# Kernel optimization log

Hardware: AMD Instinct MI355X
Metric: run time of the kernel (lower is better)

The kernel has to match this reference:

```python
import jax, jax.numpy as jnp
import numpy as np


def setup_inputs() -> dict:
    key = jax.random.key(0)
    kq, kk, kv = jax.random.split(key, 3)
    B, H, S, D = 2, 16, 2048, 64
    return {
        "queries": jax.random.normal(kq, (B, H, S, D), dtype=jnp.float32),
        "keys": jax.random.normal(kk, (B, H, S, D), dtype=jnp.float32),
        "values": jax.random.normal(kv, (B, H, S, D), dtype=jnp.float32),
        "d_k": D,
    }


def reference(queries, keys, values, d_k):
    # scores = Q K^T / sqrt(d_k)  -> [B, H, S, S]
    scale = 1.0 / jnp.sqrt(jnp.asarray(d_k, dtype=queries.dtype))
    scores = jnp.einsum("bhqd,bhkd->bhqk", queries, keys) * scale
    weights = jax.nn.softmax(scores, axis=-1)
    return jnp.einsum("bhqk,bhkd->bhqd", weights, values)
```

## Files before the change

### kernel.cpp

```cpp
#include <hip/hip_runtime.h>


typedef _Float16 half8 __attribute__((ext_vector_type(8)));
typedef _Float16 half4 __attribute__((ext_vector_type(4)));
typedef __fp16 fp16x2 __attribute__((ext_vector_type(2)));
typedef float floatx4 __attribute__((ext_vector_type(4)));

constexpr int BQ = 128;
constexpr int BK = 64;
constexpr int DH = 64;
constexpr int SLEN = 2048;
constexpr int NT = SLEN / BK;
constexpr int THREADS = 256;

#define MFMA16(a, b, c) __builtin_amdgcn_mfma_f32_16x16x32_f16(a, b, c, 0, 0, 0)

static __device__ __forceinline__ void load_lds16(const _Float16* g, _Float16* l) {
    __builtin_amdgcn_global_load_lds(
        (const __attribute__((address_space(1))) void*)g,
        (__attribute__((address_space(3))) void*)l, 16, 0, 0);
}

__global__ __launch_bounds__(256)
void prep_frags(const float* __restrict__ K, const float* __restrict__ V,
                _Float16* __restrict__ F)
{
    __shared__ _Float16 kt_[64 * 72];
    __shared__ _Float16 vt_[64 * 72];
    const int tid  = threadIdx.x;
    const int tile = blockIdx.x & 31;
    const int head = blockIdx.x >> 5;
    const size_t base = ((size_t)head * SLEN + tile * 64) * DH;
    const float4* Ks = (const float4*)(K + base);
    const float4* Vs = (const float4*)(V + base);
    #pragma unroll
    for (int r = 0; r < 4; r++) {
        int i = tid + 256 * r, row = i >> 4, g = i & 15;
        float4 a = Ks[row * 16 + g];
        half4 h;
        h[0] = (_Float16)a.x; h[1] = (_Float16)a.y;
        h[2] = (_Float16)a.z; h[3] = (_Float16)a.w;
        *(half4*)&kt_[row * 72 + g * 4] = h;
        float4 b = Vs[row * 16 + g];
        half4 h2;
        h2[0] = (_Float16)b.x; h2[1] = (_Float16)b.y;
        h2[2] = (_Float16)b.z; h2[3] = (_Float16)b.w;
        *(half4*)&vt_[row * 72 + g * 4] = h2;
    }
    __syncthreads();
    _Float16* dst = F + (size_t)(head * 32 + tile) * 8192;
    #pragma unroll
    for (int r = 0; r < 2; r++) {
        int s = tid + 256 * r;
        int frag = s >> 6, lane = s & 63;
        int kd = frag >> 2, c = frag & 3;
        int quad = lane >> 4, n16 = lane & 15;
        int key = (c >> 1) * 32 + (c & 1) * 4 + (n16 >> 2) * 8 + (n16 & 3);
        *(half8*)&dst[s * 8] = *(const half8*)&kt_[key * 72 + kd * 32 + quad * 8];
    }
    #pragma unroll
    for (int r = 0; r < 2; r++) {
        int s = tid + 256 * r;
        int frag = s >> 6, lane = s & 63;
        int kd2 = frag >> 2, c2 = frag & 3;
        int quad = lane >> 4, n16 = lane & 15;
        int d = c2 * 16 + n16;
        int key0 = kd2 * 32 + quad * 8;
        half8 h;
        #pragma unroll
        for (int j = 0; j < 8; j++) h[j] = vt_[(key0 + j) * 72 + d];
        *(half8*)&dst[4096 + s * 8] = h;
    }
}

__global__ __launch_bounds__(THREADS, 2)
void attn_f16_mfma(const float* __restrict__ Q, const _Float16* __restrict__ F,
                   float* __restrict__ Out, const int* __restrict__ dkp)
{
    __shared__ _Float16 lds[2][8192];

    const int tid  = threadIdx.x;
    const int wq   = tid >> 6;
    const int lane = tid & 63;
    const int quad = lane >> 4;
    const int n16  = lane & 15;

    const int id   = blockIdx.x;
    const int xcd  = id & 7;
    const int slot = id >> 3;
    const int head = xcd * 4 + (slot >> 4);
    const int qt   = slot & 15;

    const float scale2 = rsqrtf((float)(*dkp)) * 1.44269504088896340736f;
    const size_t headoff = (size_t)head * SLEN * DH;

    half8 qB[2][2];
    {
        const float4* Qg = (const float4*)(Q + headoff + (size_t)(qt * BQ + wq * 32) * DH);
        #pragma unroll
        for (int rg = 0; rg < 2; rg++)
            #pragma unroll
            for (int kd = 0; kd < 2; kd++) {
                int row = rg * 16 + n16;
                float4 a = Qg[row * 16 + kd * 8 + quad * 2];
                float4 b = Qg[row * 16 + kd * 8 + quad * 2 + 1];
                half8 h;
                h[0] = (_Float16)(a.x * scale2); h[1] = (_Float16)(a.y * scale2);
                h[2] = (_Float16)(a.z * scale2); h[3] = (_Float16)(a.w * scale2);
                h[4] = (_Float16)(b.x * scale2); h[5] = (_Float16)(b.y * scale2);
                h[6] = (_Float16)(b.z * scale2); h[7] = (_Float16)(b.w * scale2);
                qB[rg][kd] = h;
            }
    }

    const _Float16* Fh = F + (size_t)head * 32 * 8192;

    auto stage = [&](int b, int kt) {
        const _Float16* src = Fh + (size_t)kt * 8192 + wq * 512 + lane * 8;
        #pragma unroll
        for (int i = 0; i < 4; i++)
            load_lds16(src + i * 2048, &lds[b][wq * 512 + i * 2048]);
    };

    floatx4 oacc[2][4];
    floatx4 lsum[2];
    const floatx4 fz = {0.f, 0.f, 0.f, 0.f};
    #pragma unroll
    for (int rg = 0; rg < 2; rg++) {
        lsum[rg] = fz;
        #pragma unroll
        for (int c2 = 0; c2 < 4; c2++) oacc[rg][c2] = fz;
    }
    half8 ones;
    #pragma unroll
    for (int j = 0; j < 8; j++) ones[j] = (_Float16)1.0f;

    union PU { fp16x2 h2[4]; half8 h8; };

    stage(0, 0);

    for (int kt = 0; kt < NT; ++kt) {
        const int cur = kt & 1;
        asm volatile("s_waitcnt vmcnt(0)" ::: "memory");
        __builtin_amdgcn_sched_barrier(0);
        __syncthreads();
        if (kt + 1 < NT) stage(cur ^ 1, kt + 1);

        const _Float16* Kl = &lds[cur][0];
        const _Float16* Vl = &lds[cur][4096];

        half8 kA[2][4];
        #pragma unroll
        for (int kd = 0; kd < 2; kd++)
            #pragma unroll
            for (int c = 0; c < 4; c++)
                kA[kd][c] = *(const half8*)&Kl[((kd * 4 + c) * 64 + lane) * 8];

        floatx4 sC[2][4];
        #pragma unroll
        for (int rg = 0; rg < 2; rg++)
            #pragma unroll
            for (int c = 0; c < 4; c++) {
                floatx4 acc = MFMA16(kA[0][c], qB[rg][0], fz);
                sC[rg][c] = MFMA16(kA[1][c], qB[rg][1], acc);
            }

        half8 pB[2][2];
        #pragma unroll
        for (int rg = 0; rg < 2; rg++)
            #pragma unroll
            for (int kd2 = 0; kd2 < 2; kd2++) {
                PU u_;
                u_.h2[0] = __builtin_amdgcn_cvt_pkrtz(exp2f(sC[rg][kd2 * 2][0]),
                                                      exp2f(sC[rg][kd2 * 2][1]));
                u_.h2[1] = __builtin_amdgcn_cvt_pkrtz(exp2f(sC[rg][kd2 * 2][2]),
                                                      exp2f(sC[rg][kd2 * 2][3]));
                u_.h2[2] = __builtin_amdgcn_cvt_pkrtz(exp2f(sC[rg][kd2 * 2 + 1][0]),
                                                      exp2f(sC[rg][kd2 * 2 + 1][1]));
                u_.h2[3] = __builtin_amdgcn_cvt_pkrtz(exp2f(sC[rg][kd2 * 2 + 1][2]),
                                                      exp2f(sC[rg][kd2 * 2 + 1][3]));
                pB[rg][kd2] = u_.h8;
            }

        half8 vA[2][4];
        #pragma unroll
        for (int kd2 = 0; kd2 < 2; kd2++)
            #pragma unroll
            for (int c2 = 0; c2 < 4; c2++)
                vA[kd2][c2] = *(const half8*)&Vl[((kd2 * 4 + c2) * 64 + lane) * 8];

        __builtin_amdgcn_s_setprio(1);
        #pragma unroll
        for (int rg = 0; rg < 2; rg++) {
            lsum[rg] = MFMA16(ones, pB[rg][0], lsum[rg]);
            lsum[rg] = MFMA16(ones, pB[rg][1], lsum[rg]);
        }
        #pragma unroll
        for (int rg = 0; rg < 2; rg++)
            #pragma unroll
            for (int c2 = 0; c2 < 4; c2++) {
                oacc[rg][c2] = MFMA16(vA[0][c2], pB[rg][0], oacc[rg][c2]);
                oacc[rg][c2] = MFMA16(vA[1][c2], pB[rg][1], oacc[rg][c2]);
            }
        __builtin_amdgcn_s_setprio(0);
    }

    float* Og = Out + headoff + (size_t)(qt * BQ + wq * 32) * DH;
    #pragma unroll
    for (int rg = 0; rg < 2; rg++) {
        float inv = 1.0f / lsum[rg][0];
        #pragma unroll
        for (int c2 = 0; c2 < 4; c2++) {
            floatx4 v = oacc[rg][c2];
            float4 w = make_float4(v[0] * inv, v[1] * inv, v[2] * inv, v[3] * inv);
            *(float4*)&Og[(rg * 16 + n16) * DH + c2 * 16 + quad * 4] = w;
        }
    }
}

extern "C" void kernel_launch(void* const* d_in, const int* in_sizes, int n_in,
                              void* d_out, int out_size, void* d_ws, size_t ws_size,
                              hipStream_t stream) {
    const float* Q = (const float*)d_in[0];
    const float* K = (const float*)d_in[1];
    const float* V = (const float*)d_in[2];
    const int*  dk = (const int*)d_in[3];
    float* Out = (float*)d_out;

    const int nbh = in_sizes[0] / (SLEN * DH);

    _Float16* F = (_Float16*)d_ws;

    prep_frags<<<nbh * 32, 256, 0, stream>>>(K, V, F);

    dim3 grid(nbh * (SLEN / BQ));
    attn_f16_mfma<<<grid, THREADS, 0, stream>>>(Q, F, Out, dk);
}
```

Baseline: 144.1 us.

## Halve query tile to 64 rows, raise occupancy, unroll double-buffer loop by two

Reduces the query block from 128 to 64 rows, so each wave handles 16 query rows instead of 32. The grid doubles and the occupancy hint rises to 4 blocks per CU. The main loop is unrolled by two with fixed LDS buffer pointers, which removes the runtime buffer indexing. The cost is that each K/V tile loaded into LDS now feeds half as many MFMAs, so staging traffic and barriers per unit of compute double.

```diff
diff --git a/kernel.cpp b/kernel.cpp
--- a/kernel.cpp
+++ b/kernel.cpp
@@ -6,7 +6,7 @@
 typedef __fp16 fp16x2 __attribute__((ext_vector_type(2)));
 typedef float floatx4 __attribute__((ext_vector_type(4)));
 
-constexpr int BQ = 128;
+constexpr int BQ = 64;
 constexpr int BK = 64;
 constexpr int DH = 64;
 constexpr int SLEN = 2048;
@@ -73,7 +73,7 @@
     }
 }
 
-__global__ __launch_bounds__(THREADS, 2)
+__global__ __launch_bounds__(THREADS, 4)
 void attn_f16_mfma(const float* __restrict__ Q, const _Float16* __restrict__ F,
                    float* __restrict__ Out, const int* __restrict__ dkp)
 {
@@ -88,66 +88,52 @@
     const int id   = blockIdx.x;
     const int xcd  = id & 7;
     const int slot = id >> 3;
-    const int head = xcd * 4 + (slot >> 4);
-    const int qt   = slot & 15;
+    const int head = xcd * 4 + (slot >> 5);
+    const int qt   = slot & 31;
 
     const float scale2 = rsqrtf((float)(*dkp)) * 1.44269504088896340736f;
     const size_t headoff = (size_t)head * SLEN * DH;
 
-    half8 qB[2][2];
+    half8 qB[2];
     {
-        const float4* Qg = (const float4*)(Q + headoff + (size_t)(qt * BQ + wq * 32) * DH);
-        #pragma unroll
-        for (int rg = 0; rg < 2; rg++)
-            #pragma unroll
-            for (int kd = 0; kd < 2; kd++) {
-                int row = rg * 16 + n16;
-                float4 a = Qg[row * 16 + kd * 8 + quad * 2];
-                float4 b = Qg[row * 16 + kd * 8 + quad * 2 + 1];
-                half8 h;
-                h[0] = (_Float16)(a.x * scale2); h[1] = (_Float16)(a.y * scale2);
-                h[2] = (_Float16)(a.z * scale2); h[3] = (_Float16)(a.w * scale2);
-                h[4] = (_Float16)(b.x * scale2); h[5] = (_Float16)(b.y * scale2);
-                h[6] = (_Float16)(b.z * scale2); h[7] = (_Float16)(b.w * scale2);
-                qB[rg][kd] = h;
-            }
+        const float4* Qg = (const float4*)(Q + headoff + (size_t)(qt * BQ + wq * 16) * DH);
+        #pragma unroll
+        for (int kd = 0; kd < 2; kd++) {
+            float4 a = Qg[n16 * 16 + kd * 8 + quad * 2];
+            float4 b = Qg[n16 * 16 + kd * 8 + quad * 2 + 1];
+            half8 h;
+            h[0] = (_Float16)(a.x * scale2); h[1] = (_Float16)(a.y * scale2);
+            h[2] = (_Float16)(a.z * scale2); h[3] = (_Float16)(a.w * scale2);
+            h[4] = (_Float16)(b.x * scale2); h[5] = (_Float16)(b.y * scale2);
+            h[6] = (_Float16)(b.z * scale2); h[7] = (_Float16)(b.w * scale2);
+            qB[kd] = h;
+        }
     }
 
     const _Float16* Fh = F + (size_t)head * 32 * 8192;
 
-    auto stage = [&](int b, int kt) {
+    auto stage = [&](_Float16* dst, int kt) {
         const _Float16* src = Fh + (size_t)kt * 8192 + wq * 512 + lane * 8;
         #pragma unroll
         for (int i = 0; i < 4; i++)
-            load_lds16(src + i * 2048, &lds[b][wq * 512 + i * 2048]);
+            load_lds16(src + i * 2048, dst + wq * 512 + i * 2048);
     };
 
-    floatx4 oacc[2][4];
-    floatx4 lsum[2];
+    floatx4 oacc[4];
+    floatx4 lsum;
     const floatx4 fz = {0.f, 0.f, 0.f, 0.f};
-    #pragma unroll
-    for (int rg = 0; rg < 2; rg++) {
-        lsum[rg] = fz;
-        #pragma unroll
-        for (int c2 = 0; c2 < 4; c2++) oacc[rg][c2] = fz;
-    }
+    lsum = fz;
+    #pragma unroll
+    for (int c2 = 0; c2 < 4; c2++) oacc[c2] = fz;
     half8 ones;
     #pragma unroll
     for (int j = 0; j < 8; j++) ones[j] = (_Float16)1.0f;
 
     union PU { fp16x2 h2[4]; half8 h8; };
 
-    stage(0, 0);
-
-    for (int kt = 0; kt < NT; ++kt) {
-        const int cur = kt & 1;
-        asm volatile("s_waitcnt vmcnt(0)" ::: "memory");
-        __builtin_amdgcn_sched_barrier(0);
-        __syncthreads();
-        if (kt + 1 < NT) stage(cur ^ 1, kt + 1);
-
-        const _Float16* Kl = &lds[cur][0];
-        const _Float16* Vl = &lds[cur][4096];
+    auto tile_compute = [&](const _Float16* Bl) {
+        const _Float16* Kl = Bl;
+        const _Float16* Vl = Bl + 4096;
 
         half8 kA[2][4];
         #pragma unroll
@@ -156,31 +142,27 @@
             for (int c = 0; c < 4; c++)
                 kA[kd][c] = *(const half8*)&Kl[((kd * 4 + c) * 64 + lane) * 8];
 
-        floatx4 sC[2][4];
-        #pragma unroll
-        for (int rg = 0; rg < 2; rg++)
-            #pragma unroll
-            for (int c = 0; c < 4; c++) {
-                floatx4 acc = MFMA16(kA[0][c], qB[rg][0], fz);
-                sC[rg][c] = MFMA16(kA[1][c], qB[rg][1], acc);
-            }
-
-        half8 pB[2][2];
-        #pragma unroll
-        for (int rg = 0; rg < 2; rg++)
-            #pragma unroll
-            for (int kd2 = 0; kd2 < 2; kd2++) {
-                PU u_;
-                u_.h2[0] = __builtin_amdgcn_cvt_pkrtz(exp2f(sC[rg][kd2 * 2][0]),
-                                                      exp2f(sC[rg][kd2 * 2][1]));
-                u_.h2[1] = __builtin_amdgcn_cvt_pkrtz(exp2f(sC[rg][kd2 * 2][2]),
-                                                      exp2f(sC[rg][kd2 * 2][3]));
-                u_.h2[2] = __builtin_amdgcn_cvt_pkrtz(exp2f(sC[rg][kd2 * 2 + 1][0]),
-                                                      exp2f(sC[rg][kd2 * 2 + 1][1]));
-                u_.h2[3] = __builtin_amdgcn_cvt_pkrtz(exp2f(sC[rg][kd2 * 2 + 1][2]),
-                                                      exp2f(sC[rg][kd2 * 2 + 1][3]));
-                pB[rg][kd2] = u_.h8;
-            }
+        floatx4 sC[4];
+        #pragma unroll
+        for (int c = 0; c < 4; c++) {
+            floatx4 acc = MFMA16(kA[0][c], qB[0], fz);
+            sC[c] = MFMA16(kA[1][c], qB[1], acc);
+        }
+
+        half8 pB[2];
+        #pragma unroll
+        for (int kd2 = 0; kd2 < 2; kd2++) {
+            PU u_;
+            u_.h2[0] = __builtin_amdgcn_cvt_pkrtz(exp2f(sC[kd2 * 2][0]),
+                                                  exp2f(sC[kd2 * 2][1]));
+            u_.h2[1] = __builtin_amdgcn_cvt_pkrtz(exp2f(sC[kd2 * 2][2]),
+                                                  exp2f(sC[kd2 * 2][3]));
+            u_.h2[2] = __builtin_amdgcn_cvt_pkrtz(exp2f(sC[kd2 * 2 + 1][0]),
+                                                  exp2f(sC[kd2 * 2 + 1][1]));
+            u_.h2[3] = __builtin_amdgcn_cvt_pkrtz(exp2f(sC[kd2 * 2 + 1][2]),
+                                                  exp2f(sC[kd2 * 2 + 1][3]));
+            pB[kd2] = u_.h8;
+        }
 
         half8 vA[2][4];
         #pragma unroll
@@ -190,31 +172,39 @@
                 vA[kd2][c2] = *(const half8*)&Vl[((kd2 * 4 + c2) * 64 + lane) * 8];
 
         __builtin_amdgcn_s_setprio(1);
-        #pragma unroll
-        for (int rg = 0; rg < 2; rg++) {
-            lsum[rg] = MFMA16(ones, pB[rg][0], lsum[rg]);
-            lsum[rg] = MFMA16(ones, pB[rg][1], lsum[rg]);
-        }
-        #pragma unroll
-        for (int rg = 0; rg < 2; rg++)
-            #pragma unroll
-            for (int c2 = 0; c2 < 4; c2++) {
-                oacc[rg][c2] = MFMA16(vA[0][c2], pB[rg][0], oacc[rg][c2]);
-                oacc[rg][c2] = MFMA16(vA[1][c2], pB[rg][1], oacc[rg][c2]);
-            }
+        lsum = MFMA16(ones, pB[0], lsum);
+        lsum = MFMA16(ones, pB[1], lsum);
+        #pragma unroll
+        for (int c2 = 0; c2 < 4; c2++) {
+            oacc[c2] = MFMA16(vA[0][c2], pB[0], oacc[c2]);
+            oacc[c2] = MFMA16(vA[1][c2], pB[1], oacc[c2]);
+        }
         __builtin_amdgcn_s_setprio(0);
-    }
-
-    float* Og = Out + headoff + (size_t)(qt * BQ + wq * 32) * DH;
-    #pragma unroll
-    for (int rg = 0; rg < 2; rg++) {
-        float inv = 1.0f / lsum[rg][0];
-        #pragma unroll
-        for (int c2 = 0; c2 < 4; c2++) {
-            floatx4 v = oacc[rg][c2];
-            float4 w = make_float4(v[0] * inv, v[1] * inv, v[2] * inv, v[3] * inv);
-            *(float4*)&Og[(rg * 16 + n16) * DH + c2 * 16 + quad * 4] = w;
-        }
+    };
+
+    stage(&lds[0][0], 0);
+
+    for (int kt = 0; kt < NT; kt += 2) {
+        asm volatile("s_waitcnt vmcnt(0)" ::: "memory");
+        __builtin_amdgcn_sched_barrier(0);
+        __syncthreads();
+        if (kt + 1 < NT) stage(&lds[1][0], kt + 1);
+        tile_compute(&lds[0][0]);
+
+        asm volatile("s_waitcnt vmcnt(0)" ::: "memory");
+        __builtin_amdgcn_sched_barrier(0);
+        __syncthreads();
+        if (kt + 2 < NT) stage(&lds[0][0], kt + 2);
+        tile_compute(&lds[1][0]);
+    }
+
+    float* Og = Out + headoff + (size_t)(qt * BQ + wq * 16) * DH;
+    float inv = 1.0f / lsum[0];
+    #pragma unroll
+    for (int c2 = 0; c2 < 4; c2++) {
+        floatx4 v = oacc[c2];
+        float4 w = make_float4(v[0] * inv, v[1] * inv, v[2] * inv, v[3] * inv);
+        *(float4*)&Og[n16 * DH + c2 * 16 + quad * 4] = w;
     }
 }
 
```

New measurement: 144.3 us. Within noise of the previous version (+0.1%).
